# Kernel optimization log

Measured on AMD Instinct MI355X. Metric: run time of the kernel, lower is better.

## Reference

```python
import jax, jax.numpy as jnp
import numpy as np

B, F, S, D = 256, 8, 200, 64
H = 36  # hidden units per field
EPS = 1e-3  # Dice BN epsilon


def setup_inputs() -> dict:
    key0 = jax.random.key(0)
    ks = jax.random.split(key0, 8)
    query = jax.random.normal(ks[0], (B, F, D), dtype=jnp.float32)
    key = jax.random.normal(ks[1], (B, F, S, D), dtype=jnp.float32)
    sequence_num = jax.random.randint(ks[2], (B, F), 1, S + 1, dtype=jnp.int32)
    W_h = jax.random.normal(ks[3], (F, 3 * D, H), dtype=jnp.float32) * 0.05
    b_h = jnp.zeros((F, H), dtype=jnp.float32)
    alpha = jnp.zeros((F,), dtype=jnp.float32)
    W_o = jax.random.normal(ks[4], (F, H, 1), dtype=jnp.float32) * 0.05
    b_o = jnp.zeros((F, 1), dtype=jnp.float32)
    return {"query": query, "key": key, "W_h": W_h, "b_h": b_h,
            "alpha": alpha, "W_o": W_o, "b_o": b_o,
            "sequence_num": sequence_num, "training": 1}


def reference(query, key, W_h, b_h, alpha, W_o, b_o, sequence_num, training):
    # query: [B,F,D], key: [B,F,S,D]
    q = query[:, :, None, :]                      # broadcast instead of tile
    qb = jnp.broadcast_to(q, key.shape)           # [B,F,S,D]
    cat = jnp.concatenate([key, qb, q - key], axis=-1)  # [B,F,S,3D]
    # per-field Dense(36), vectorized across fields
    h = jnp.einsum('bfsc,fch->bfsh', cat, W_h) + b_h[None, :, None, :]
    # Dice: BatchNorm (no affine, training-mode batch stats over batch+seq per field/feature)
    mean = h.mean(axis=(0, 2), keepdims=True)
    var = h.var(axis=(0, 2), keepdims=True)
    p = jax.nn.sigmoid((h - mean) * jax.lax.rsqrt(var + EPS))
    h = (alpha[None, :, None, None] * (1.0 - p) + p) * h
    # per-field Dense(1) -> attention scores [B,F,S]
    scores = jnp.einsum('bfsh,fh->bfs', h, W_o[:, :, 0]) + b_o[None, :, 0, None]
    # mask invalid positions and softmax over sequence
    mask = jnp.arange(key.shape[2])[None, None, :] < sequence_num[:, :, None]
    scores = jnp.where(mask, scores, -jnp.inf)
    attn = jax.nn.softmax(scores, axis=-1)        # [B,F,S]
    # weighted sum over sequence -> [B,F,D]
    return jnp.einsum('bfs,bfsd->bfd', attn, key)
```

## Files before the change

kernel.cpp:

```cpp
#include <hip/hip_runtime.h>
#include <math.h>

#define NB 256
#define NF 8
#define NS 200
#define ND 64
#define NH 36
#define MT 13
#define EPSV 1e-3f

#define WS_SUM 0
#define WS_SQ  288
#define WS_QT  1152
#define WS_WK  (1152 + 2048 * 48)

typedef __attribute__((ext_vector_type(8))) short short8;
typedef __attribute__((ext_vector_type(4))) float f32x4;

__device__ __forceinline__ unsigned short f32_to_bf16(float x) {
    unsigned u = __float_as_uint(x);
    unsigned r = u + 0x7FFFu + ((u >> 16) & 1u);
    return (unsigned short)(r >> 16);
}
__device__ __forceinline__ float bf16_to_f32(unsigned short h) {
    return __uint_as_float(((unsigned)h) << 16);
}
__device__ __forceinline__ short8 cvt8(float4 a, float4 b) {
    short8 r;
    r[0] = (short)f32_to_bf16(a.x); r[1] = (short)f32_to_bf16(a.y);
    r[2] = (short)f32_to_bf16(a.z); r[3] = (short)f32_to_bf16(a.w);
    r[4] = (short)f32_to_bf16(b.x); r[5] = (short)f32_to_bf16(b.y);
    r[6] = (short)f32_to_bf16(b.z); r[7] = (short)f32_to_bf16(b.w);
    return r;
}

__global__ __launch_bounds__(256) void k_prep(
    const float* __restrict__ query, const float* __restrict__ W_h,
    const float* __restrict__ b_h, float* __restrict__ ws)
{
    const int blk = blockIdx.x, tid = threadIdx.x;
    if (blk < NB) {
        __shared__ float qs[NF * ND];
        for (int i = tid; i < NF * ND; i += 256)
            qs[i] = query[(size_t)blk * NF * ND + i];
        __syncthreads();
        for (int i = tid; i < NF * 48; i += 256) {
            int f = i / 48, h = i - f * 48;
            float acc = 0.f;
            if (h < NH) {
                const float* Wf = W_h + (size_t)f * (3 * ND * NH);
                acc = b_h[f * NH + h];
                for (int d = 0; d < ND; ++d)
                    acc += qs[f * ND + d] * (Wf[(ND + d) * NH + h] + Wf[(2 * ND + d) * NH + h]);
            }
            ws[WS_QT + (size_t)(blk * NF + f) * 48 + h] = acc;
        }
    } else {
        const int f = blk - NB;
        const float* Wf = W_h + (size_t)f * (3 * ND * NH);
        unsigned short* wk = (unsigned short*)(ws + WS_WK) + f * (48 * ND);
        for (int i = tid; i < 48 * ND; i += 256) {
            int h = i >> 6, d = i & 63;
            float v = (h < NH) ? (Wf[d * NH + h] - Wf[(2 * ND + d) * NH + h]) : 0.f;
            wk[h * ND + d] = f32_to_bf16(v);
        }
    }
}

__global__ __launch_bounds__(256, 4) void k_stats(
    const float* __restrict__ key, float* __restrict__ ws)
{
    const int blk = blockIdx.x;
    const int f = blk & (NF - 1);
    const int tid = threadIdx.x;
    const int lane = tid & 63;
    const int wv = tid >> 6;
    const int col = lane & 15;
    const int quad = lane >> 4;

    __shared__ float sumP[48], sqP[48];
    if (tid < 48) { sumP[tid] = 0.f; sqP[tid] = 0.f; }
    __syncthreads();

    const float* kbase = key + (size_t)blk * (NS * ND);
    const unsigned short* wk = (const unsigned short*)(ws + WS_WK) + f * (48 * ND);

    short8 bfr[3][2];
    float qv[3];
    #pragma unroll
    for (int nt = 0; nt < 3; ++nt) {
        #pragma unroll
        for (int ks = 0; ks < 2; ++ks)
            bfr[nt][ks] = *(const short8*)&wk[(nt * 16 + col) * ND + ks * 32 + quad * 8];
        qv[nt] = ws[WS_QT + (size_t)blk * 48 + nt * 16 + col];
    }

    float s_sum[3] = {0.f, 0.f, 0.f}, s_sq[3] = {0.f, 0.f, 0.f};
    for (int mt = wv; mt < MT; mt += 4) {
        const int s = 16 * mt + col;
        const float4* p = (const float4*)(kbase + (size_t)(s < NS ? s : NS - 1) * ND + quad * 8);
        float4 a0 = p[0], a1 = p[1];
        float4 b0 = p[8], b1 = p[9];
        short8 ah0 = cvt8(a0, a1);
        short8 ah1 = cvt8(b0, b1);
        #pragma unroll
        for (int nt = 0; nt < 3; ++nt) {
            f32x4 acc = {qv[nt], qv[nt], qv[nt], qv[nt]};
            acc = __builtin_amdgcn_mfma_f32_16x16x32_bf16(ah0, bfr[nt][0], acc, 0, 0, 0);
            acc = __builtin_amdgcn_mfma_f32_16x16x32_bf16(ah1, bfr[nt][1], acc, 0, 0, 0);
            #pragma unroll
            for (int r = 0; r < 4; ++r) {
                int srow = 16 * mt + quad * 4 + r;
                if (srow < NS) { float v = acc[r]; s_sum[nt] += v; s_sq[nt] += v * v; }
            }
        }
    }
    #pragma unroll
    for (int nt = 0; nt < 3; ++nt) {
        float sv = s_sum[nt], qq = s_sq[nt];
        sv += __shfl_xor(sv, 16, 64); sv += __shfl_xor(sv, 32, 64);
        qq += __shfl_xor(qq, 16, 64); qq += __shfl_xor(qq, 32, 64);
        if (quad == 0) {
            atomicAdd(&sumP[nt * 16 + col], sv);
            atomicAdd(&sqP[nt * 16 + col], qq);
        }
    }
    __syncthreads();
    if (tid < NH) {
        atomicAdd(&ws[WS_SUM + f * NH + tid], sumP[tid]);
        atomicAdd(&ws[WS_SQ + f * NH + tid], sqP[tid]);
    }
}

__global__ __launch_bounds__(256, 3) void k_attn(
    const float* __restrict__ key, const float* __restrict__ alpha,
    const float* __restrict__ W_o, const float* __restrict__ b_o,
    const int* __restrict__ seqn, const float* __restrict__ ws,
    float* __restrict__ out)
{
    const int blk = blockIdx.x;
    const int f = blk & (NF - 1);
    const int tid = threadIdx.x;
    const int lane = tid & 63;
    const int wv = tid >> 6;
    const int col = lane & 15;
    const int quad = lane >> 4;

    __shared__ float sw[208];
    __shared__ float redM[4], redS[4];
    __shared__ float pout[4][64];

    const float* kbase = key + (size_t)blk * (NS * ND);
    const unsigned short* wk = (const unsigned short*)(ws + WS_WK) + f * (48 * ND);
    const float inv_n = 1.f / (float)(NB * NS);

    short8 bfr[3][2];
    float qv[3], mn[3], iv[3], wo[3];
    #pragma unroll
    for (int nt = 0; nt < 3; ++nt) {
        #pragma unroll
        for (int ks = 0; ks < 2; ++ks)
            bfr[nt][ks] = *(const short8*)&wk[(nt * 16 + col) * ND + ks * 32 + quad * 8];
        const int hh = nt * 16 + col;
        const bool hv = hh < NH;
        const int hc = hv ? hh : 0;
        qv[nt] = ws[WS_QT + (size_t)blk * 48 + hh];
        const float sm = ws[WS_SUM + f * NH + hc];
        const float sq = ws[WS_SQ + f * NH + hc];
        const float m = sm * inv_n;
        mn[nt] = m;
        iv[nt] = rsqrtf(fmaxf(sq * inv_n - m * m, 0.f) + EPSV);
        wo[nt] = hv ? W_o[f * NH + hh] : 0.f;
    }
    const float alf = alpha[f];
    const float bo = b_o[f];
    const int sq_n = seqn[blk];

    short8 kah[4][2];
    #pragma unroll
    for (int t = 0; t < 4; ++t) {
        const int mt = wv + 4 * t;
        if (mt < MT) {
            const int s = 16 * mt + col;
            const float4* p = (const float4*)(kbase + (size_t)(s < NS ? s : NS - 1) * ND + quad * 8);
            float4 a0 = p[0], a1 = p[1];
            float4 b0 = p[8], b1 = p[9];
            kah[t][0] = cvt8(a0, a1);
            kah[t][1] = cvt8(b0, b1);
            float part[4] = {0.f, 0.f, 0.f, 0.f};
            #pragma unroll
            for (int nt = 0; nt < 3; ++nt) {
                f32x4 acc = {qv[nt], qv[nt], qv[nt], qv[nt]};
                acc = __builtin_amdgcn_mfma_f32_16x16x32_bf16(kah[t][0], bfr[nt][0], acc, 0, 0, 0);
                acc = __builtin_amdgcn_mfma_f32_16x16x32_bf16(kah[t][1], bfr[nt][1], acc, 0, 0, 0);
                #pragma unroll
                for (int r = 0; r < 4; ++r) {
                    const float h = acc[r];
                    const float pg = 1.f / (1.f + __expf(-(h - mn[nt]) * iv[nt]));
                    part[r] += (alf + (1.f - alf) * pg) * h * wo[nt];
                }
            }
            #pragma unroll
            for (int r = 0; r < 4; ++r) {
                float v = part[r];
                v += __shfl_xor(v, 1, 64);
                v += __shfl_xor(v, 2, 64);
                v += __shfl_xor(v, 4, 64);
                v += __shfl_xor(v, 8, 64);
                const int srow = 16 * mt + quad * 4 + r;
                if (col == 0 && srow < NS) sw[srow] = v + bo;
            }
        }
    }
    __syncthreads();

    const bool valid = (tid < 208) && (tid < sq_n);
    const float sc = valid ? sw[tid] : -1e30f;
    float m = sc;
    m = fmaxf(m, __shfl_xor(m, 1, 64));  m = fmaxf(m, __shfl_xor(m, 2, 64));
    m = fmaxf(m, __shfl_xor(m, 4, 64));  m = fmaxf(m, __shfl_xor(m, 8, 64));
    m = fmaxf(m, __shfl_xor(m, 16, 64)); m = fmaxf(m, __shfl_xor(m, 32, 64));
    if (lane == 0) redM[wv] = m;
    __syncthreads();
    const float maxv = fmaxf(fmaxf(redM[0], redM[1]), fmaxf(redM[2], redM[3]));
    const float e = valid ? __expf(sc - maxv) : 0.f;
    float l = e;
    l += __shfl_xor(l, 1, 64);  l += __shfl_xor(l, 2, 64);
    l += __shfl_xor(l, 4, 64);  l += __shfl_xor(l, 8, 64);
    l += __shfl_xor(l, 16, 64); l += __shfl_xor(l, 32, 64);
    if (lane == 0) redS[wv] = l;
    __syncthreads();
    const float isum = 1.f / (redS[0] + redS[1] + redS[2] + redS[3]);
    if (tid < 208) sw[tid] = e * isum;
    __syncthreads();

    float po0[8] = {0,0,0,0,0,0,0,0}, po1[8] = {0,0,0,0,0,0,0,0};
    #pragma unroll
    for (int t = 0; t < 4; ++t) {
        const int mt = wv + 4 * t;
        if (mt < MT) {
            const float w = sw[16 * mt + col];
            #pragma unroll
            for (int j = 0; j < 8; ++j) {
                po0[j] += w * bf16_to_f32((unsigned short)kah[t][0][j]);
                po1[j] += w * bf16_to_f32((unsigned short)kah[t][1][j]);
            }
        }
    }
    #pragma unroll
    for (int off = 1; off <= 8; off <<= 1) {
        #pragma unroll
        for (int j = 0; j < 8; ++j) {
            po0[j] += __shfl_xor(po0[j], off, 64);
            po1[j] += __shfl_xor(po1[j], off, 64);
        }
    }
    if (col == 0) {
        #pragma unroll
        for (int j = 0; j < 8; ++j) {
            pout[wv][quad * 8 + j] = po0[j];
            pout[wv][32 + quad * 8 + j] = po1[j];
        }
    }
    __syncthreads();
    if (tid < 64)
        out[(size_t)blk * ND + tid] =
            pout[0][tid] + pout[1][tid] + pout[2][tid] + pout[3][tid];
}

extern "C" void kernel_launch(void* const* d_in, const int* in_sizes, int n_in,
                              void* d_out, int out_size, void* d_ws, size_t ws_size,
                              hipStream_t stream) {
    const float* query = (const float*)d_in[0];
    const float* key   = (const float*)d_in[1];
    const float* W_h   = (const float*)d_in[2];
    const float* b_h   = (const float*)d_in[3];
    const float* alpha = (const float*)d_in[4];
    const float* W_o   = (const float*)d_in[5];
    const float* b_o   = (const float*)d_in[6];
    const int*   seqn  = (const int*)d_in[7];
    float* out = (float*)d_out;
    float* ws  = (float*)d_ws;

    hipMemsetAsync(ws, 0, 576 * sizeof(float), stream);
    k_prep<<<NB + NF, 256, 0, stream>>>(query, W_h, b_h, ws);
    k_stats<<<NB * NF, 256, 0, stream>>>(key, ws);
    k_attn<<<NB * NF, 256, 0, stream>>>(key, alpha, W_o, b_o, seqn, ws, out);
}
```

Before: 211.1 us.

## Fuse query projection into stats kernel, drop memset, reload key in attn

Replaces the separate hipMemsetAsync with zeroing done inside the prep kernel. Prep now only precomputes the summed W2+W3 weights. The per-(batch,field) query projection moves into k_stats, which computes it in shared memory and writes it to the workspace for k_attn. k_attn no longer keeps the bf16 key fragments in registers; it reloads fp32 key for the weighted sum and raises launch bounds to 4 blocks per SM. This trades an extra key read, likely served from cache, for lower register pressure and higher occupancy, and uses full-precision key values in the output sum.

```diff
diff --git a/kernel.cpp b/kernel.cpp
--- a/kernel.cpp
+++ b/kernel.cpp
@@ -13,6 +13,7 @@
 #define WS_SQ  288
 #define WS_QT  1152
 #define WS_WK  (1152 + 2048 * 48)
+#define WS_W23 (WS_WK + (NF * 48 * ND) / 2)
 
 typedef __attribute__((ext_vector_type(8))) short short8;
 typedef __attribute__((ext_vector_type(4))) float f32x4;
@@ -21,9 +22,6 @@
     unsigned u = __float_as_uint(x);
     unsigned r = u + 0x7FFFu + ((u >> 16) & 1u);
     return (unsigned short)(r >> 16);
-}
-__device__ __forceinline__ float bf16_to_f32(unsigned short h) {
-    return __uint_as_float(((unsigned)h) << 16);
 }
 __device__ __forceinline__ short8 cvt8(float4 a, float4 b) {
     short8 r;
@@ -35,28 +33,11 @@
 }
 
 __global__ __launch_bounds__(256) void k_prep(
-    const float* __restrict__ query, const float* __restrict__ W_h,
-    const float* __restrict__ b_h, float* __restrict__ ws)
+    const float* __restrict__ W_h, float* __restrict__ ws)
 {
     const int blk = blockIdx.x, tid = threadIdx.x;
-    if (blk < NB) {
-        __shared__ float qs[NF * ND];
-        for (int i = tid; i < NF * ND; i += 256)
-            qs[i] = query[(size_t)blk * NF * ND + i];
-        __syncthreads();
-        for (int i = tid; i < NF * 48; i += 256) {
-            int f = i / 48, h = i - f * 48;
-            float acc = 0.f;
-            if (h < NH) {
-                const float* Wf = W_h + (size_t)f * (3 * ND * NH);
-                acc = b_h[f * NH + h];
-                for (int d = 0; d < ND; ++d)
-                    acc += qs[f * ND + d] * (Wf[(ND + d) * NH + h] + Wf[(2 * ND + d) * NH + h]);
-            }
-            ws[WS_QT + (size_t)(blk * NF + f) * 48 + h] = acc;
-        }
-    } else {
-        const int f = blk - NB;
+    if (blk < NF) {
+        const int f = blk;
         const float* Wf = W_h + (size_t)f * (3 * ND * NH);
         unsigned short* wk = (unsigned short*)(ws + WS_WK) + f * (48 * ND);
         for (int i = tid; i < 48 * ND; i += 256) {
@@ -64,11 +45,19 @@
             float v = (h < NH) ? (Wf[d * NH + h] - Wf[(2 * ND + d) * NH + h]) : 0.f;
             wk[h * ND + d] = f32_to_bf16(v);
         }
+        float* w23 = ws + WS_W23 + f * (ND * 48);
+        for (int i = tid; i < ND * 48; i += 256) {
+            int d = i / 48, h = i - d * 48;
+            w23[i] = (h < NH) ? (Wf[(ND + d) * NH + h] + Wf[(2 * ND + d) * NH + h]) : 0.f;
+        }
+    } else {
+        for (int i = tid; i < 576; i += 256) ws[i] = 0.f;
     }
 }
 
 __global__ __launch_bounds__(256, 4) void k_stats(
-    const float* __restrict__ key, float* __restrict__ ws)
+    const float* __restrict__ query, const float* __restrict__ key,
+    const float* __restrict__ b_h, float* __restrict__ ws)
 {
     const int blk = blockIdx.x;
     const int f = blk & (NF - 1);
@@ -79,7 +68,21 @@
     const int quad = lane >> 4;
 
     __shared__ float sumP[48], sqP[48];
+    __shared__ float qsh[ND];
+    __shared__ float qt_sh[48];
     if (tid < 48) { sumP[tid] = 0.f; sqP[tid] = 0.f; }
+    if (tid < ND) qsh[tid] = query[(size_t)blk * ND + tid];
+    __syncthreads();
+
+    if (tid < 48) {
+        const int h = tid;
+        float acc = (h < NH) ? b_h[f * NH + h] : 0.f;
+        const float* w23 = ws + WS_W23 + f * (ND * 48);
+        #pragma unroll 8
+        for (int d = 0; d < ND; ++d) acc += qsh[d] * w23[d * 48 + h];
+        qt_sh[h] = acc;
+        ws[WS_QT + (size_t)blk * 48 + h] = acc;
+    }
     __syncthreads();
 
     const float* kbase = key + (size_t)blk * (NS * ND);
@@ -92,7 +95,7 @@
         #pragma unroll
         for (int ks = 0; ks < 2; ++ks)
             bfr[nt][ks] = *(const short8*)&wk[(nt * 16 + col) * ND + ks * 32 + quad * 8];
-        qv[nt] = ws[WS_QT + (size_t)blk * 48 + nt * 16 + col];
+        qv[nt] = qt_sh[nt * 16 + col];
     }
 
     float s_sum[3] = {0.f, 0.f, 0.f}, s_sq[3] = {0.f, 0.f, 0.f};
@@ -132,7 +135,7 @@
     }
 }
 
-__global__ __launch_bounds__(256, 3) void k_attn(
+__global__ __launch_bounds__(256, 4) void k_attn(
     const float* __restrict__ key, const float* __restrict__ alpha,
     const float* __restrict__ W_o, const float* __restrict__ b_o,
     const int* __restrict__ seqn, const float* __restrict__ ws,
@@ -176,7 +179,6 @@
     const float bo = b_o[f];
     const int sq_n = seqn[blk];
 
-    short8 kah[4][2];
     #pragma unroll
     for (int t = 0; t < 4; ++t) {
         const int mt = wv + 4 * t;
@@ -185,14 +187,14 @@
             const float4* p = (const float4*)(kbase + (size_t)(s < NS ? s : NS - 1) * ND + quad * 8);
             float4 a0 = p[0], a1 = p[1];
             float4 b0 = p[8], b1 = p[9];
-            kah[t][0] = cvt8(a0, a1);
-            kah[t][1] = cvt8(b0, b1);
+            short8 ah0 = cvt8(a0, a1);
+            short8 ah1 = cvt8(b0, b1);
             float part[4] = {0.f, 0.f, 0.f, 0.f};
             #pragma unroll
             for (int nt = 0; nt < 3; ++nt) {
                 f32x4 acc = {qv[nt], qv[nt], qv[nt], qv[nt]};
-                acc = __builtin_amdgcn_mfma_f32_16x16x32_bf16(kah[t][0], bfr[nt][0], acc, 0, 0, 0);
-                acc = __builtin_amdgcn_mfma_f32_16x16x32_bf16(kah[t][1], bfr[nt][1], acc, 0, 0, 0);
+                acc = __builtin_amdgcn_mfma_f32_16x16x32_bf16(ah0, bfr[nt][0], acc, 0, 0, 0);
+                acc = __builtin_amdgcn_mfma_f32_16x16x32_bf16(ah1, bfr[nt][1], acc, 0, 0, 0);
                 #pragma unroll
                 for (int r = 0; r < 4; ++r) {
                     const float h = acc[r];
@@ -239,12 +241,15 @@
     for (int t = 0; t < 4; ++t) {
         const int mt = wv + 4 * t;
         if (mt < MT) {
+            const int s = 16 * mt + col;
             const float w = sw[16 * mt + col];
-            #pragma unroll
-            for (int j = 0; j < 8; ++j) {
-                po0[j] += w * bf16_to_f32((unsigned short)kah[t][0][j]);
-                po1[j] += w * bf16_to_f32((unsigned short)kah[t][1][j]);
-            }
+            const float4* p = (const float4*)(kbase + (size_t)(s < NS ? s : NS - 1) * ND + quad * 8);
+            float4 a0 = p[0], a1 = p[1];
+            float4 b0 = p[8], b1 = p[9];
+            po0[0] += w * a0.x; po0[1] += w * a0.y; po0[2] += w * a0.z; po0[3] += w * a0.w;
+            po0[4] += w * a1.x; po0[5] += w * a1.y; po0[6] += w * a1.z; po0[7] += w * a1.w;
+            po1[0] += w * b0.x; po1[1] += w * b0.y; po1[2] += w * b0.z; po1[3] += w * b0.w;
+            po1[4] += w * b1.x; po1[5] += w * b1.y; po1[6] += w * b1.z; po1[7] += w * b1.w;
         }
     }
     #pragma unroll
@@ -282,8 +287,7 @@
     float* out = (float*)d_out;
     float* ws  = (float*)d_ws;
 
-    hipMemsetAsync(ws, 0, 576 * sizeof(float), stream);
-    k_prep<<<NB + NF, 256, 0, stream>>>(query, W_h, b_h, ws);
-    k_stats<<<NB * NF, 256, 0, stream>>>(key, ws);
+    k_prep<<<NF + 1, 256, 0, stream>>>(W_h, ws);
+    k_stats<<<NB * NF, 256, 0, stream>>>(query, key, b_h, ws);
     k_attn<<<NB * NF, 256, 0, stream>>>(key, alpha, W_o, b_o, seqn, ws, out);
 }
```

Result: slower. 221.9 us (+5.1%).

## Front-load all key loads in stats/attn kernels and fold memset into prep kernel

Applied to the files above, without the earlier changes.

Both key-reading kernels now issue all of a wave's global loads up front into registers before any MFMA work, so the memory requests can be in flight together instead of one loop iteration at a time. The workspace zeroing memset is replaced by an extra block in the prep kernel, which removes one launch. The stats kernel's occupancy hint is lowered from 4 to 3 to make room for the larger register footprint, trading occupancy for memory-level parallelism.

```diff
diff --git a/kernel.cpp b/kernel.cpp
--- a/kernel.cpp
+++ b/kernel.cpp
@@ -39,10 +39,22 @@
     const float* __restrict__ b_h, float* __restrict__ ws)
 {
     const int blk = blockIdx.x, tid = threadIdx.x;
-    if (blk < NB) {
+    if (blk < NF) {
+        const int f = blk;
+        const float* Wf = W_h + (size_t)f * (3 * ND * NH);
+        unsigned short* wk = (unsigned short*)(ws + WS_WK) + f * (48 * ND);
+        for (int i = tid; i < 48 * ND; i += 256) {
+            int h = i >> 6, d = i & 63;
+            float v = (h < NH) ? (Wf[d * NH + h] - Wf[(2 * ND + d) * NH + h]) : 0.f;
+            wk[h * ND + d] = f32_to_bf16(v);
+        }
+    } else if (blk == NF) {
+        for (int i = tid; i < 576; i += 256) ws[i] = 0.f;
+    } else {
+        const int b = blk - NF - 1;
         __shared__ float qs[NF * ND];
         for (int i = tid; i < NF * ND; i += 256)
-            qs[i] = query[(size_t)blk * NF * ND + i];
+            qs[i] = query[(size_t)b * NF * ND + i];
         __syncthreads();
         for (int i = tid; i < NF * 48; i += 256) {
             int f = i / 48, h = i - f * 48;
@@ -53,21 +65,12 @@
                 for (int d = 0; d < ND; ++d)
                     acc += qs[f * ND + d] * (Wf[(ND + d) * NH + h] + Wf[(2 * ND + d) * NH + h]);
             }
-            ws[WS_QT + (size_t)(blk * NF + f) * 48 + h] = acc;
-        }
-    } else {
-        const int f = blk - NB;
-        const float* Wf = W_h + (size_t)f * (3 * ND * NH);
-        unsigned short* wk = (unsigned short*)(ws + WS_WK) + f * (48 * ND);
-        for (int i = tid; i < 48 * ND; i += 256) {
-            int h = i >> 6, d = i & 63;
-            float v = (h < NH) ? (Wf[d * NH + h] - Wf[(2 * ND + d) * NH + h]) : 0.f;
-            wk[h * ND + d] = f32_to_bf16(v);
-        }
-    }
-}
-
-__global__ __launch_bounds__(256, 4) void k_stats(
+            ws[WS_QT + (size_t)(b * NF + f) * 48 + h] = acc;
+        }
+    }
+}
+
+__global__ __launch_bounds__(256, 3) void k_stats(
     const float* __restrict__ key, float* __restrict__ ws)
 {
     const int blk = blockIdx.x;
@@ -85,6 +88,18 @@
     const float* kbase = key + (size_t)blk * (NS * ND);
     const unsigned short* wk = (const unsigned short*)(ws + WS_WK) + f * (48 * ND);
 
+    float4 pf[4][4];
+    #pragma unroll
+    for (int t = 0; t < 4; ++t) {
+        const int mt = wv + 4 * t;
+        if (mt < MT) {
+            const int s = 16 * mt + col;
+            const float4* p = (const float4*)(kbase + (size_t)(s < NS ? s : NS - 1) * ND + quad * 8);
+            pf[t][0] = p[0]; pf[t][1] = p[1];
+            pf[t][2] = p[8]; pf[t][3] = p[9];
+        }
+    }
+
     short8 bfr[3][2];
     float qv[3];
     #pragma unroll
@@ -96,22 +111,22 @@
     }
 
     float s_sum[3] = {0.f, 0.f, 0.f}, s_sq[3] = {0.f, 0.f, 0.f};
-    for (int mt = wv; mt < MT; mt += 4) {
-        const int s = 16 * mt + col;
-        const float4* p = (const float4*)(kbase + (size_t)(s < NS ? s : NS - 1) * ND + quad * 8);
-        float4 a0 = p[0], a1 = p[1];
-        float4 b0 = p[8], b1 = p[9];
-        short8 ah0 = cvt8(a0, a1);
-        short8 ah1 = cvt8(b0, b1);
-        #pragma unroll
-        for (int nt = 0; nt < 3; ++nt) {
-            f32x4 acc = {qv[nt], qv[nt], qv[nt], qv[nt]};
-            acc = __builtin_amdgcn_mfma_f32_16x16x32_bf16(ah0, bfr[nt][0], acc, 0, 0, 0);
-            acc = __builtin_amdgcn_mfma_f32_16x16x32_bf16(ah1, bfr[nt][1], acc, 0, 0, 0);
+    #pragma unroll
+    for (int t = 0; t < 4; ++t) {
+        const int mt = wv + 4 * t;
+        if (mt < MT) {
+            short8 ah0 = cvt8(pf[t][0], pf[t][1]);
+            short8 ah1 = cvt8(pf[t][2], pf[t][3]);
             #pragma unroll
-            for (int r = 0; r < 4; ++r) {
-                int srow = 16 * mt + quad * 4 + r;
-                if (srow < NS) { float v = acc[r]; s_sum[nt] += v; s_sq[nt] += v * v; }
+            for (int nt = 0; nt < 3; ++nt) {
+                f32x4 acc = {qv[nt], qv[nt], qv[nt], qv[nt]};
+                acc = __builtin_amdgcn_mfma_f32_16x16x32_bf16(ah0, bfr[nt][0], acc, 0, 0, 0);
+                acc = __builtin_amdgcn_mfma_f32_16x16x32_bf16(ah1, bfr[nt][1], acc, 0, 0, 0);
+                #pragma unroll
+                for (int r = 0; r < 4; ++r) {
+                    int srow = 16 * mt + quad * 4 + r;
+                    if (srow < NS) { float v = acc[r]; s_sum[nt] += v; s_sq[nt] += v * v; }
+                }
             }
         }
     }
@@ -154,6 +169,28 @@
     const unsigned short* wk = (const unsigned short*)(ws + WS_WK) + f * (48 * ND);
     const float inv_n = 1.f / (float)(NB * NS);
 
+    short8 kah[4][2];
+    {
+        float4 pf[4][4];
+        const float4 z4 = {0.f, 0.f, 0.f, 0.f};
+        pf[3][0] = z4; pf[3][1] = z4; pf[3][2] = z4; pf[3][3] = z4;
+        #pragma unroll
+        for (int t = 0; t < 4; ++t) {
+            const int mt = wv + 4 * t;
+            if (mt < MT) {
+                const int s = 16 * mt + col;
+                const float4* p = (const float4*)(kbase + (size_t)(s < NS ? s : NS - 1) * ND + quad * 8);
+                pf[t][0] = p[0]; pf[t][1] = p[1];
+                pf[t][2] = p[8]; pf[t][3] = p[9];
+            }
+        }
+        #pragma unroll
+        for (int t = 0; t < 4; ++t) {
+            kah[t][0] = cvt8(pf[t][0], pf[t][1]);
+            kah[t][1] = cvt8(pf[t][2], pf[t][3]);
+        }
+    }
+
     short8 bfr[3][2];
     float qv[3], mn[3], iv[3], wo[3];
     #pragma unroll
@@ -176,17 +213,10 @@
     const float bo = b_o[f];
     const int sq_n = seqn[blk];
 
-    short8 kah[4][2];
     #pragma unroll
     for (int t = 0; t < 4; ++t) {
         const int mt = wv + 4 * t;
         if (mt < MT) {
-            const int s = 16 * mt + col;
-            const float4* p = (const float4*)(kbase + (size_t)(s < NS ? s : NS - 1) * ND + quad * 8);
-            float4 a0 = p[0], a1 = p[1];
-            float4 b0 = p[8], b1 = p[9];
-            kah[t][0] = cvt8(a0, a1);
-            kah[t][1] = cvt8(b0, b1);
             float part[4] = {0.f, 0.f, 0.f, 0.f};
             #pragma unroll
             for (int nt = 0; nt < 3; ++nt) {
@@ -282,8 +312,7 @@
     float* out = (float*)d_out;
     float* ws  = (float*)d_ws;
 
-    hipMemsetAsync(ws, 0, 576 * sizeof(float), stream);
-    k_prep<<<NB + NF, 256, 0, stream>>>(query, W_h, b_h, ws);
+    k_prep<<<NB + NF + 1, 256, 0, stream>>>(query, W_h, b_h, ws);
     k_stats<<<NB * NF, 256, 0, stream>>>(key, ws);
     k_attn<<<NB * NF, 256, 0, stream>>>(key, alpha, W_o, b_o, seqn, ws, out);
 }
```

Result: no change. 210.7 us (median of 2 runs) (-0.2%).
